# Optimization experiments

Hardware: AMD Instinct MI355X
Metric: run time of the kernel (lower is better)

## Reference

```python
import jax, jax.numpy as jnp
import numpy as np

N = 50000
E = 800000
IN_CH = 128
HID = 64
HEADS = 4
OUT_CH = 64
NEG_SLOPE = 0.2


def add_self_loops(edge_index, num_nodes):
    loops = jnp.arange(num_nodes, dtype=edge_index.dtype)
    src = jnp.concatenate([edge_index[0], loops])
    dst = jnp.concatenate([edge_index[1], loops])
    return src, dst


def gat_layer(x, src, dst, W, a_src, a_dst, b, heads, out_ch, concat):
    n = x.shape[0]
    h = (x @ W).reshape(n, heads, out_ch)              # [N,H,C]
    al_src = jnp.einsum('nhc,hc->nh', h, a_src)        # [N,H]
    al_dst = jnp.einsum('nhc,hc->nh', h, a_dst)        # [N,H]
    e = jax.nn.leaky_relu(al_src[src] + al_dst[dst], NEG_SLOPE)  # [Et,H]
    # segment softmax over incoming edges of each destination node
    m = jax.ops.segment_max(e, dst, num_segments=n)
    ex = jnp.exp(e - m[dst])
    denom = jax.ops.segment_sum(ex, dst, num_segments=n)
    alpha = ex / (denom[dst] + 1e-16)                  # [Et,H]
    msg = h[src] * alpha[:, :, None]                   # [Et,H,C]
    out = jax.ops.segment_sum(msg, dst, num_segments=n)  # [N,H,C]
    if concat:
        out = out.reshape(n, heads * out_ch)
    else:
        out = out.mean(axis=1)
    return out + b


def setup_inputs() -> dict:
    key = jax.random.key(0)
    ks = jax.random.split(key, 10)
    x = jax.random.normal(ks[0], (N, IN_CH), dtype=jnp.float32)
    edge_index = jax.random.randint(ks[1], (2, E), 0, N, dtype=jnp.int64)
    s1 = 1.0 / np.sqrt(IN_CH)
    W1 = jax.random.normal(ks[2], (IN_CH, HEADS * HID), dtype=jnp.float32) * s1
    a_src1 = jax.random.normal(ks[3], (HEADS, HID), dtype=jnp.float32) * 0.1
    a_dst1 = jax.random.normal(ks[4], (HEADS, HID), dtype=jnp.float32) * 0.1
    b1 = jnp.zeros((HEADS * HID,), dtype=jnp.float32)
    s2 = 1.0 / np.sqrt(HEADS * HID)
    W2 = jax.random.normal(ks[5], (HEADS * HID, OUT_CH), dtype=jnp.float32) * s2
    a_src2 = jax.random.normal(ks[6], (1, OUT_CH), dtype=jnp.float32) * 0.1
    a_dst2 = jax.random.normal(ks[7], (1, OUT_CH), dtype=jnp.float32) * 0.1
    b2 = jnp.zeros((OUT_CH,), dtype=jnp.float32)
    return {"x": x, "edge_index": edge_index, "W1": W1, "a_src1": a_src1,
            "a_dst1": a_dst1, "b1": b1, "W2": W2, "a_src2": a_src2,
            "a_dst2": a_dst2, "b2": b2}


def reference(x, edge_index, W1, a_src1, a_dst1, b1, W2, a_src2, a_dst2, b2):
    src, dst = add_self_loops(edge_index, x.shape[0])
    h = gat_layer(x, src, dst, W1, a_src1, a_dst1, b1, HEADS, HID, True)
    h = jax.nn.elu(h)
    h = gat_layer(h, src, dst, W2, a_src2, a_dst2, b2, 1, OUT_CH, False)
    return jax.nn.elu(h)
```

## Files before the change

### kernel.cpp

```cpp
#include <hip/hip_runtime.h>
#include <hip/hip_bf16.h>
#include <cstdint>
#include <cstddef>


typedef float f32x4 __attribute__((ext_vector_type(4)));
typedef __fp16 f16x8 __attribute__((ext_vector_type(8)));
typedef __fp16 f16x4 __attribute__((ext_vector_type(4)));

static __device__ __forceinline__ float lrelu02(float x) { return x > 0.f ? x : 0.2f * x; }
static __device__ __forceinline__ float eluf(float x)    { return x > 0.f ? x : __expf(x) - 1.f; }

__global__ void detect_kernel(const int* __restrict__ ei, int* __restrict__ flag, int e) {
    if (blockIdx.x == 0 && threadIdx.x == 0) {
        int zeros = 0;
        int m = e < 64 ? e : 64;
        for (int i = 0; i < m; ++i) if (ei[2 * i + 1] == 0) ++zeros;
        *flag = (zeros >= (m / 2 + 1)) ? 1 : 0;
    }
}

__global__ void convert_hist_kernel(const int* __restrict__ ei, const int* __restrict__ flag,
                                    int* __restrict__ es, int* __restrict__ deg, int e) {
    int i = blockIdx.x * 256 + threadIdx.x;
    if (i < e) {
        int f = *flag;
        int s = f ? ei[2 * i] : ei[i];
        int d = f ? ei[2 * (e + i)] : ei[e + i];
        es[i] = s;
        es[e + i] = d;
        atomicAdd(&deg[d], 1);
    }
}

__global__ __launch_bounds__(256) void scan_blocks_kernel(const int* __restrict__ deg,
                                                          int* __restrict__ loc,
                                                          int* __restrict__ bsum, int n) {
    __shared__ int wsum[4];
    int t = threadIdx.x, lane = t & 63, w = t >> 6;
    int base = blockIdx.x * 1024 + t * 4;
    int4 v = make_int4(0, 0, 0, 0);
    if (base + 3 < n) {
        v = *(const int4*)(deg + base);
        v.x += 1; v.y += 1; v.z += 1; v.w += 1;
    } else {
        if (base < n) v.x = deg[base] + 1;
        if (base + 1 < n) v.y = deg[base + 1] + 1;
        if (base + 2 < n) v.z = deg[base + 2] + 1;
        if (base + 3 < n) v.w = deg[base + 3] + 1;
    }
    int s = v.x + v.y + v.z + v.w;
    int incl = s;
    #pragma unroll
    for (int d = 1; d < 64; d <<= 1) { int o = __shfl_up(incl, d); if (lane >= d) incl += o; }
    if (lane == 63) wsum[w] = incl;
    __syncthreads();
    int woff = 0;
    for (int k = 0; k < w; ++k) woff += wsum[k];
    int excl = woff + incl - s;
    if (base < n) {
        int e0 = excl, e1 = e0 + v.x, e2 = e1 + v.y, e3 = e2 + v.z;
        loc[base] = e0;
        if (base + 1 < n) loc[base + 1] = e1;
        if (base + 2 < n) loc[base + 2] = e2;
        if (base + 3 < n) loc[base + 3] = e3;
    }
    if (t == 255) bsum[blockIdx.x] = woff + incl;
}

__global__ __launch_bounds__(256) void scan_sums_kernel(const int* __restrict__ bsum,
                                                        int* __restrict__ boff, int nb,
                                                        int* __restrict__ rowptr, int n) {
    __shared__ int ws[4];
    int t = threadIdx.x, lane = t & 63, w = t >> 6;
    int v = (t < nb) ? bsum[t] : 0;
    int incl = v;
    #pragma unroll
    for (int d = 1; d < 64; d <<= 1) { int o = __shfl_up(incl, d); if (lane >= d) incl += o; }
    if (lane == 63) ws[w] = incl;
    __syncthreads();
    int woff = 0;
    for (int k = 0; k < w; ++k) woff += ws[k];
    int excl = woff + incl - v;
    if (t < nb) boff[t] = excl;
    if (t == nb - 1) rowptr[n] = excl + v;
}

__global__ void scan_add_kernel(int* __restrict__ rowptr, const int* __restrict__ boff,
                                int* __restrict__ cursor, int n) {
    int i = blockIdx.x * 256 + threadIdx.x;
    if (i < n) {
        int v = rowptr[i] + boff[i >> 10];
        rowptr[i] = v;
        cursor[i] = v;
    }
}

__global__ void scatter_kernel(const int* __restrict__ src, const int* __restrict__ dst,
                               int* __restrict__ cursor, int* __restrict__ sidx,
                               int e, int et) {
    int i = blockIdx.x * blockDim.x + threadIdx.x;
    if (i < et) {
        int d, s;
        if (i < e) { d = dst[i]; s = src[i]; } else { d = s = i - e; }
        int pos = atomicAdd(&cursor[d], 1);
        sidx[pos] = s;
    }
}

__global__ __launch_bounds__(256) void gemm1_kernel(const float* __restrict__ A,
                                                    const float* __restrict__ B,
                                                    __fp16* __restrict__ C,
                                                    const float* __restrict__ a_src,
                                                    const float* __restrict__ a_dst,
                                                    float* __restrict__ als,
                                                    float* __restrict__ ald, int M) {
    constexpr int N = 256, K = 128;
    __shared__ __fp16 sm[17920];
    #define AS(r, c)  sm[(r) * 40 + (c)]
    #define BST(r, c) sm[2560 + (r) * 40 + (c)]
    #define CS(r, c)  sm[(r) * 264 + (c)]
    float* sa = (float*)(sm + 16896);
    float* sd = (float*)(sm + 17408);
    int t = threadIdx.x;
    int wv = t >> 6, l = t & 63;
    int lm = l & 15, kq = l >> 4;
    int bm = blockIdx.x * 64;
    sa[t] = a_src[t];
    sd[t] = a_dst[t];
    f32x4 zero = {0.f, 0.f, 0.f, 0.f};
    f32x4 acc[4][4] = {{zero, zero, zero, zero}, {zero, zero, zero, zero},
                       {zero, zero, zero, zero}, {zero, zero, zero, zero}};
    int arow = t >> 2, achunk = (t & 3) * 8;
    for (int k0 = 0; k0 < K; k0 += 32) {
        {
            int gr = bm + arow;
            f16x8 av;
            if (gr < M) {
                float4 a0 = *(const float4*)(A + (size_t)gr * K + k0 + achunk);
                float4 a1 = *(const float4*)(A + (size_t)gr * K + k0 + achunk + 4);
                av[0] = (__fp16)a0.x; av[1] = (__fp16)a0.y; av[2] = (__fp16)a0.z; av[3] = (__fp16)a0.w;
                av[4] = (__fp16)a1.x; av[5] = (__fp16)a1.y; av[6] = (__fp16)a1.z; av[7] = (__fp16)a1.w;
            } else { f16x8 z = {0,0,0,0,0,0,0,0}; av = z; }
            *(f16x8*)&AS(arow, achunk) = av;
        }
        {
            #pragma unroll
            for (int bc = 0; bc < 4; ++bc) {
                f16x8 bh;
                #pragma unroll
                for (int j = 0; j < 8; ++j)
                    bh[j] = (__fp16)B[(size_t)(k0 + bc * 8 + j) * N + t];
                *(f16x8*)&BST(t, bc * 8) = bh;
            }
        }
        __syncthreads();
        #pragma unroll
        for (int nt = 0; nt < 4; ++nt) {
            f16x8 bfrag = *(const f16x8*)&BST(wv * 64 + nt * 16 + lm, kq * 8);
            #pragma unroll
            for (int mt = 0; mt < 4; ++mt) {
                f16x8 afrag = *(const f16x8*)&AS(mt * 16 + lm, kq * 8);
                acc[mt][nt] = __builtin_amdgcn_mfma_f32_16x16x32_f16(afrag, bfrag, acc[mt][nt], 0, 0, 0);
            }
        }
        __syncthreads();
    }
    #pragma unroll
    for (int mt = 0; mt < 4; ++mt)
        #pragma unroll
        for (int nt = 0; nt < 4; ++nt)
            #pragma unroll
            for (int r = 0; r < 4; ++r)
                CS(mt * 16 + kq * 4 + r, wv * 64 + nt * 16 + lm) = (__fp16)acc[mt][nt][r];
    __syncthreads();
    {
        int row = t >> 2, head = t & 3;
        int gr = bm + row;
        f16x8 c[8];
        #pragma unroll
        for (int q = 0; q < 8; ++q) c[q] = *(const f16x8*)&CS(row, head * 64 + q * 8);
        float ps = 0.f, pd = 0.f;
        #pragma unroll
        for (int q = 0; q < 8; ++q)
            #pragma unroll
            for (int j = 0; j < 8; ++j) {
                float v = (float)c[q][j];
                ps += v * sa[head * 64 + q * 8 + j];
                pd += v * sd[head * 64 + q * 8 + j];
            }
        if (gr < M) {
            f16x8* gp = (f16x8*)(C + (size_t)gr * 256 + head * 64);
            #pragma unroll
            for (int q = 0; q < 8; ++q) gp[q] = c[q];
            als[gr * 4 + head] = ps;
            ald[gr * 4 + head] = pd;
        }
    }
    #undef AS
    #undef BST
    #undef CS
}

__global__ __launch_bounds__(256) void gemm2_kernel(const __fp16* __restrict__ A,
                                                    const float* __restrict__ B,
                                                    __fp16* __restrict__ C,
                                                    const float* __restrict__ a_src,
                                                    const float* __restrict__ a_dst,
                                                    float* __restrict__ als,
                                                    float* __restrict__ ald,
                                                    int M, int N, int K) {
    __shared__ __fp16 sm[5120];
    #define AS(r, c)  sm[(r) * 40 + (c)]
    #define BST(r, c) sm[2560 + (r) * 40 + (c)]
    #define CS(r, c)  sm[(r) * 72 + (c)]
    int t = threadIdx.x;
    int wv = t >> 6, l = t & 63;
    int bm = blockIdx.x * 64;
    int lm = l & 15, kq = l >> 4;
    f32x4 zero = {0.f, 0.f, 0.f, 0.f};
    f32x4 acc[4] = {zero, zero, zero, zero};
    int arow = t >> 2, achunk = (t & 3) * 8;
    int bnn = t & 63, bkc = (t >> 6) * 8;
    for (int k0 = 0; k0 < K; k0 += 32) {
        {
            int gr = bm + arow;
            f16x8 av;
            if (gr < M) av = *(const f16x8*)(A + (size_t)gr * K + k0 + achunk);
            else { f16x8 z = {0,0,0,0,0,0,0,0}; av = z; }
            *(f16x8*)&AS(arow, achunk) = av;
        }
        {
            f16x8 bh;
            #pragma unroll
            for (int j = 0; j < 8; ++j)
                bh[j] = (__fp16)B[(size_t)(k0 + bkc + j) * N + bnn];
            *(f16x8*)&BST(bnn, bkc) = bh;
        }
        __syncthreads();
        f16x8 bfrag = *(const f16x8*)&BST(wv * 16 + lm, kq * 8);
        #pragma unroll
        for (int mt = 0; mt < 4; ++mt) {
            f16x8 afrag = *(const f16x8*)&AS(mt * 16 + lm, kq * 8);
            acc[mt] = __builtin_amdgcn_mfma_f32_16x16x32_f16(afrag, bfrag, acc[mt], 0, 0, 0);
        }
        __syncthreads();
    }
    #pragma unroll
    for (int mt = 0; mt < 4; ++mt)
        #pragma unroll
        for (int r = 0; r < 4; ++r)
            CS(mt * 16 + kq * 4 + r, wv * 16 + lm) = (__fp16)acc[mt][r];
    __syncthreads();
    {
        int row = t >> 2, ch = (t & 3) * 16;
        int gr = bm + row;
        f16x8 c0 = *(const f16x8*)&CS(row, ch);
        f16x8 c1 = *(const f16x8*)&CS(row, ch + 8);
        if (gr < M) {
            f16x8* gp = (f16x8*)(C + (size_t)gr * N + ch);
            gp[0] = c0; gp[1] = c1;
        }
        float ps = 0.f, pd = 0.f;
        #pragma unroll
        for (int j = 0; j < 8; ++j) {
            float v0 = (float)c0[j], v1 = (float)c1[j];
            ps += v0 * a_src[ch + j] + v1 * a_src[ch + 8 + j];
            pd += v0 * a_dst[ch + j] + v1 * a_dst[ch + 8 + j];
        }
        ps += __shfl_down(ps, 2); ps += __shfl_down(ps, 1);
        pd += __shfl_down(pd, 2); pd += __shfl_down(pd, 1);
        if ((t & 3) == 0 && gr < M) {
            als[gr] = ps;
            ald[gr] = pd;
        }
    }
    #undef AS
    #undef BST
    #undef CS
}

__global__ __launch_bounds__(256) void agg1_kernel(const __fp16* __restrict__ h1,
                                                   const int* __restrict__ sidx,
                                                   const int* __restrict__ rowptr,
                                                   const float* __restrict__ als,
                                                   const float* __restrict__ ald,
                                                   const float* __restrict__ b1,
                                                   __fp16* __restrict__ x2, int n) {
    int t = threadIdx.x, wv = t >> 6, l = t & 63;
    int node = blockIdx.x * 4 + wv;
    if (node >= n) return;
    int le = l & 31, halfE = l >> 5;
    int head = le >> 3;
    float aldn = ald[node * 4 + head];
    int p0 = rowptr[node], p1 = rowptr[node + 1];
    float acc[8] = {0.f, 0.f, 0.f, 0.f, 0.f, 0.f, 0.f, 0.f};
    float accw = 0.f;
    auto body = [&](int p) {
        int s = sidx[p];
        float wt = __expf(lrelu02(als[s * 4 + head] + aldn));
        accw += wt;
        f16x8 r = *(const f16x8*)(h1 + (size_t)s * 256 + le * 8);
        #pragma unroll
        for (int j = 0; j < 8; ++j) acc[j] += wt * (float)r[j];
    };
    int p = p0 + halfE;
    for (; p + 2 < p1; p += 4) { body(p); body(p + 2); }
    if (p < p1) body(p);
    #pragma unroll
    for (int j = 0; j < 8; ++j) acc[j] += __shfl_down(acc[j], 32);
    accw += __shfl_down(accw, 32);
    if (l < 32) {
        float rd = 1.f / (accw + 1e-16f);
        f16x8 o;
        #pragma unroll
        for (int j = 0; j < 8; ++j) {
            float v = acc[j] * rd + b1[le * 8 + j];
            o[j] = (__fp16)eluf(v);
        }
        *(f16x8*)(x2 + (size_t)node * 256 + le * 8) = o;
    }
}

__global__ __launch_bounds__(256) void agg2_kernel(const __fp16* __restrict__ h2,
                                                   const int* __restrict__ sidx,
                                                   const int* __restrict__ rowptr,
                                                   const float* __restrict__ als,
                                                   const float* __restrict__ ald,
                                                   const float* __restrict__ b2,
                                                   float* __restrict__ out, int n) {
    int t = threadIdx.x, wv = t >> 6, l = t & 63;
    int node = blockIdx.x * 4 + wv;
    if (node >= n) return;
    int slot = l >> 3, cq = l & 7;
    float aldn = ald[node];
    int p0 = rowptr[node], p1 = rowptr[node + 1];
    float acc[8] = {0.f, 0.f, 0.f, 0.f, 0.f, 0.f, 0.f, 0.f};
    float accw = 0.f;
    auto body = [&](int p) {
        int s = sidx[p];
        float wt = __expf(lrelu02(als[s] + aldn));
        accw += wt;
        f16x8 r = *(const f16x8*)(h2 + (size_t)s * 64 + cq * 8);
        #pragma unroll
        for (int j = 0; j < 8; ++j) acc[j] += wt * (float)r[j];
    };
    int p = p0 + slot;
    for (; p + 8 < p1; p += 16) { body(p); body(p + 8); }
    if (p < p1) body(p);
    #pragma unroll
    for (int j = 0; j < 8; ++j) {
        acc[j] += __shfl_down(acc[j], 32);
        acc[j] += __shfl_down(acc[j], 16);
        acc[j] += __shfl_down(acc[j], 8);
    }
    accw += __shfl_down(accw, 32);
    accw += __shfl_down(accw, 16);
    accw += __shfl_down(accw, 8);
    if (l < 8) {
        float rd = 1.f / (accw + 1e-16f);
        float4 o0, o1;
        o0.x = eluf(acc[0] * rd + b2[cq * 8 + 0]);
        o0.y = eluf(acc[1] * rd + b2[cq * 8 + 1]);
        o0.z = eluf(acc[2] * rd + b2[cq * 8 + 2]);
        o0.w = eluf(acc[3] * rd + b2[cq * 8 + 3]);
        o1.x = eluf(acc[4] * rd + b2[cq * 8 + 4]);
        o1.y = eluf(acc[5] * rd + b2[cq * 8 + 5]);
        o1.z = eluf(acc[6] * rd + b2[cq * 8 + 6]);
        o1.w = eluf(acc[7] * rd + b2[cq * 8 + 7]);
        float4* gp = (float4*)(out + (size_t)node * 64 + cq * 8);
        gp[0] = o0; gp[1] = o1;
    }
}

extern "C" void kernel_launch(void* const* d_in, const int* in_sizes, int n_in,
                              void* d_out, int out_size, void* d_ws, size_t ws_size,
                              hipStream_t stream) {
    const float* x   = (const float*)d_in[0];
    const int*   ei  = (const int*)d_in[1];
    const float* W1  = (const float*)d_in[2];
    const float* as1 = (const float*)d_in[3];
    const float* ad1 = (const float*)d_in[4];
    const float* b1  = (const float*)d_in[5];
    const float* W2  = (const float*)d_in[6];
    const float* as2 = (const float*)d_in[7];
    const float* ad2 = (const float*)d_in[8];
    const float* b2  = (const float*)d_in[9];
    float* out = (float*)d_out;

    const int n  = in_sizes[0] / 128;
    const int e  = in_sizes[1] / 2;
    const int et = e + n;

    char* w = (char*)d_ws;
    size_t off = 0;
    auto take = [&](size_t bytes) -> void* {
        void* p = w + off;
        off = (off + bytes + 255) & ~(size_t)255;
        return p;
    };
    __fp16* h1h = (__fp16*)take((size_t)n * 256 * 2);
    __fp16* x2h = (__fp16*)take((size_t)n * 256 * 2);
    __fp16* h2h = (__fp16*)take((size_t)n * 64 * 2);
    float* al1s = (float*)take((size_t)n * 4 * 4);
    float* al1d = (float*)take((size_t)n * 4 * 4);
    float* al2s = (float*)take((size_t)n * 4);
    float* al2d = (float*)take((size_t)n * 4);
    int* deg    = (int*)take((size_t)(n + 1) * 4);
    int* rowptr = (int*)take((size_t)(n + 1) * 4);
    int* cursor = (int*)take((size_t)(n + 1) * 4);
    int* sidx   = (int*)take((size_t)et * 4);
    int* es     = (int*)take((size_t)2 * e * 4);
    int* bsum   = (int*)take(1024);
    int* boff   = (int*)take(1024);
    int* flag   = (int*)take(256);

    detect_kernel<<<1, 64, 0, stream>>>(ei, flag, e);
    hipMemsetAsync(deg, 0, (size_t)n * 4, stream);
    convert_hist_kernel<<<(e + 255) / 256, 256, 0, stream>>>(ei, flag, es, deg, e);
    const int* srcA = es;
    const int* dstA = es + e;

    int nb = (n + 1023) / 1024;
    scan_blocks_kernel<<<nb, 256, 0, stream>>>(deg, rowptr, bsum, n);
    scan_sums_kernel<<<1, 256, 0, stream>>>(bsum, boff, nb, rowptr, n);
    scan_add_kernel<<<(n + 255) / 256, 256, 0, stream>>>(rowptr, boff, cursor, n);
    scatter_kernel<<<(et + 255) / 256, 256, 0, stream>>>(srcA, dstA, cursor, sidx, e, et);

    const int mblocks = (n + 63) / 64;
    const int nodeblocks = (n + 3) / 4;

    gemm1_kernel<<<mblocks, 256, 0, stream>>>(x, W1, h1h, as1, ad1, al1s, al1d, n);
    agg1_kernel<<<nodeblocks, 256, 0, stream>>>(h1h, sidx, rowptr, al1s, al1d, b1, x2h, n);

    gemm2_kernel<<<mblocks, 256, 0, stream>>>(x2h, W2, h2h, as2, ad2, al2s, al2d, n, 64, 256);
    agg2_kernel<<<nodeblocks, 256, 0, stream>>>(h2h, sidx, rowptr, al2s, al2d, b2, out, n);
}
```

Baseline: 311.7 us.

## Pre-transpose weights to fp16, drop edge copy, widen GEMM K-tiles, unroll agg1

Adds a prep kernel that transposes and converts W1/W2 to fp16 once, so the GEMM kernels load B with contiguous vector loads instead of strided scalar float reads. Removes the intermediate es edge-array copy: the histogram and scatter kernels read edge_index directly using the layout flag. Doubles the GEMM K-tile to 64, halving the number of sync rounds, and unrolls the agg1 edge loop by 4. The detect kernel becomes a wave ballot. The extra launch and larger shared memory may reduce occupancy.

```diff
diff --git a/kernel.cpp b/kernel.cpp
--- a/kernel.cpp
+++ b/kernel.cpp
@@ -12,23 +12,19 @@
 static __device__ __forceinline__ float eluf(float x)    { return x > 0.f ? x : __expf(x) - 1.f; }
 
 __global__ void detect_kernel(const int* __restrict__ ei, int* __restrict__ flag, int e) {
-    if (blockIdx.x == 0 && threadIdx.x == 0) {
-        int zeros = 0;
-        int m = e < 64 ? e : 64;
-        for (int i = 0; i < m; ++i) if (ei[2 * i + 1] == 0) ++zeros;
-        *flag = (zeros >= (m / 2 + 1)) ? 1 : 0;
-    }
-}
-
-__global__ void convert_hist_kernel(const int* __restrict__ ei, const int* __restrict__ flag,
-                                    int* __restrict__ es, int* __restrict__ deg, int e) {
+    int lane = threadIdx.x;
+    int m = e < 64 ? e : 64;
+    int z = (lane < m && ei[2 * lane + 1] == 0) ? 1 : 0;
+    unsigned long long bal = __ballot(z);
+    if (lane == 0) *flag = (__popcll(bal) >= m / 2 + 1) ? 1 : 0;
+}
+
+__global__ void hist_kernel(const int* __restrict__ ei, const int* __restrict__ flag,
+                            int* __restrict__ deg, int e) {
     int i = blockIdx.x * 256 + threadIdx.x;
     if (i < e) {
         int f = *flag;
-        int s = f ? ei[2 * i] : ei[i];
         int d = f ? ei[2 * (e + i)] : ei[e + i];
-        es[i] = s;
-        es[e + i] = d;
         atomicAdd(&deg[d], 1);
     }
 }
@@ -96,32 +92,47 @@
     }
 }
 
-__global__ void scatter_kernel(const int* __restrict__ src, const int* __restrict__ dst,
+__global__ void scatter_kernel(const int* __restrict__ ei, const int* __restrict__ flag,
                                int* __restrict__ cursor, int* __restrict__ sidx,
                                int e, int et) {
-    int i = blockIdx.x * blockDim.x + threadIdx.x;
-    if (i < et) {
-        int d, s;
-        if (i < e) { d = dst[i]; s = src[i]; } else { d = s = i - e; }
-        int pos = atomicAdd(&cursor[d], 1);
-        sidx[pos] = s;
+    int i = blockIdx.x * 256 + threadIdx.x;
+    if (i >= et) return;
+    int s, d;
+    if (i < e) {
+        int f = *flag;
+        s = f ? ei[2 * i] : ei[i];
+        d = f ? ei[2 * (e + i)] : ei[e + i];
+    } else { s = d = i - e; }
+    int pos = atomicAdd(&cursor[d], 1);
+    sidx[pos] = s;
+}
+
+__global__ void prep_kernel(const float* __restrict__ W1, const float* __restrict__ W2,
+                            __fp16* __restrict__ w1t, __fp16* __restrict__ w2t) {
+    int i = blockIdx.x * 256 + threadIdx.x;
+    if (i < 32768) {
+        int nn = i >> 7, k = i & 127;
+        w1t[i] = (__fp16)W1[k * 256 + nn];
+    } else {
+        int j = i - 32768;
+        int nn = j >> 8, k = j & 255;
+        w2t[j] = (__fp16)W2[k * 64 + nn];
     }
 }
 
 __global__ __launch_bounds__(256) void gemm1_kernel(const float* __restrict__ A,
-                                                    const float* __restrict__ B,
+                                                    const __fp16* __restrict__ w1t,
                                                     __fp16* __restrict__ C,
                                                     const float* __restrict__ a_src,
                                                     const float* __restrict__ a_dst,
                                                     float* __restrict__ als,
                                                     float* __restrict__ ald, int M) {
-    constexpr int N = 256, K = 128;
-    __shared__ __fp16 sm[17920];
-    #define AS(r, c)  sm[(r) * 40 + (c)]
-    #define BST(r, c) sm[2560 + (r) * 40 + (c)]
+    __shared__ __fp16 sm[24064];
+    #define AS(r, c)  sm[(r) * 72 + (c)]
+    #define BST(r, c) sm[4608 + (r) * 72 + (c)]
     #define CS(r, c)  sm[(r) * 264 + (c)]
-    float* sa = (float*)(sm + 16896);
-    float* sd = (float*)(sm + 17408);
+    float* sa = (float*)(sm + 23040);
+    float* sd = (float*)(sm + 23552);
     int t = threadIdx.x;
     int wv = t >> 6, l = t & 63;
     int lm = l & 15, kq = l >> 4;
@@ -131,37 +142,46 @@
     f32x4 zero = {0.f, 0.f, 0.f, 0.f};
     f32x4 acc[4][4] = {{zero, zero, zero, zero}, {zero, zero, zero, zero},
                        {zero, zero, zero, zero}, {zero, zero, zero, zero}};
-    int arow = t >> 2, achunk = (t & 3) * 8;
-    for (int k0 = 0; k0 < K; k0 += 32) {
+    int arow = t >> 2, akp = (t & 3) * 16;
+    for (int k0 = 0; k0 < 128; k0 += 64) {
         {
             int gr = bm + arow;
-            f16x8 av;
+            f16x8 av0, av1;
             if (gr < M) {
-                float4 a0 = *(const float4*)(A + (size_t)gr * K + k0 + achunk);
-                float4 a1 = *(const float4*)(A + (size_t)gr * K + k0 + achunk + 4);
-                av[0] = (__fp16)a0.x; av[1] = (__fp16)a0.y; av[2] = (__fp16)a0.z; av[3] = (__fp16)a0.w;
-                av[4] = (__fp16)a1.x; av[5] = (__fp16)a1.y; av[6] = (__fp16)a1.z; av[7] = (__fp16)a1.w;
-            } else { f16x8 z = {0,0,0,0,0,0,0,0}; av = z; }
-            *(f16x8*)&AS(arow, achunk) = av;
+                const float* ap = A + (size_t)gr * 128 + k0 + akp;
+                float4 a0 = *(const float4*)(ap + 0);
+                float4 a1 = *(const float4*)(ap + 4);
+                float4 a2 = *(const float4*)(ap + 8);
+                float4 a3 = *(const float4*)(ap + 12);
+                av0[0] = (__fp16)a0.x; av0[1] = (__fp16)a0.y; av0[2] = (__fp16)a0.z; av0[3] = (__fp16)a0.w;
+                av0[4] = (__fp16)a1.x; av0[5] = (__fp16)a1.y; av0[6] = (__fp16)a1.z; av0[7] = (__fp16)a1.w;
+                av1[0] = (__fp16)a2.x; av1[1] = (__fp16)a2.y; av1[2] = (__fp16)a2.z; av1[3] = (__fp16)a2.w;
+                av1[4] = (__fp16)a3.x; av1[5] = (__fp16)a3.y; av1[6] = (__fp16)a3.z; av1[7] = (__fp16)a3.w;
+            } else {
+                f16x8 z = {0,0,0,0,0,0,0,0}; av0 = z; av1 = z;
+            }
+            *(f16x8*)&AS(arow, akp) = av0;
+            *(f16x8*)&AS(arow, akp + 8) = av1;
         }
         {
-            #pragma unroll
-            for (int bc = 0; bc < 4; ++bc) {
-                f16x8 bh;
+            const __fp16* bp = w1t + (size_t)t * 128 + k0;
+            #pragma unroll
+            for (int c = 0; c < 8; ++c)
+                *(f16x8*)&BST(t, c * 8) = *(const f16x8*)(bp + c * 8);
+        }
+        __syncthreads();
+        #pragma unroll
+        for (int ki = 0; ki < 2; ++ki) {
+            int kc = ki * 32 + kq * 8;
+            f16x8 af[4];
+            #pragma unroll
+            for (int mt = 0; mt < 4; ++mt) af[mt] = *(const f16x8*)&AS(mt * 16 + lm, kc);
+            #pragma unroll
+            for (int nt = 0; nt < 4; ++nt) {
+                f16x8 bfrag = *(const f16x8*)&BST(wv * 64 + nt * 16 + lm, kc);
                 #pragma unroll
-                for (int j = 0; j < 8; ++j)
-                    bh[j] = (__fp16)B[(size_t)(k0 + bc * 8 + j) * N + t];
-                *(f16x8*)&BST(t, bc * 8) = bh;
-            }
-        }
-        __syncthreads();
-        #pragma unroll
-        for (int nt = 0; nt < 4; ++nt) {
-            f16x8 bfrag = *(const f16x8*)&BST(wv * 64 + nt * 16 + lm, kq * 8);
-            #pragma unroll
-            for (int mt = 0; mt < 4; ++mt) {
-                f16x8 afrag = *(const f16x8*)&AS(mt * 16 + lm, kq * 8);
-                acc[mt][nt] = __builtin_amdgcn_mfma_f32_16x16x32_f16(afrag, bfrag, acc[mt][nt], 0, 0, 0);
+                for (int mt = 0; mt < 4; ++mt)
+                    acc[mt][nt] = __builtin_amdgcn_mfma_f32_16x16x32_f16(af[mt], bfrag, acc[mt][nt], 0, 0, 0);
             }
         }
         __syncthreads();
@@ -203,46 +223,51 @@
 }
 
 __global__ __launch_bounds__(256) void gemm2_kernel(const __fp16* __restrict__ A,
-                                                    const float* __restrict__ B,
+                                                    const __fp16* __restrict__ w2t,
                                                     __fp16* __restrict__ C,
                                                     const float* __restrict__ a_src,
                                                     const float* __restrict__ a_dst,
                                                     float* __restrict__ als,
-                                                    float* __restrict__ ald,
-                                                    int M, int N, int K) {
-    __shared__ __fp16 sm[5120];
-    #define AS(r, c)  sm[(r) * 40 + (c)]
-    #define BST(r, c) sm[2560 + (r) * 40 + (c)]
+                                                    float* __restrict__ ald, int M) {
+    __shared__ __fp16 sm[9216];
+    #define AS(r, c)  sm[(r) * 72 + (c)]
+    #define BST(r, c) sm[4608 + (r) * 72 + (c)]
     #define CS(r, c)  sm[(r) * 72 + (c)]
     int t = threadIdx.x;
     int wv = t >> 6, l = t & 63;
+    int lm = l & 15, kq = l >> 4;
     int bm = blockIdx.x * 64;
-    int lm = l & 15, kq = l >> 4;
     f32x4 zero = {0.f, 0.f, 0.f, 0.f};
     f32x4 acc[4] = {zero, zero, zero, zero};
-    int arow = t >> 2, achunk = (t & 3) * 8;
-    int bnn = t & 63, bkc = (t >> 6) * 8;
-    for (int k0 = 0; k0 < K; k0 += 32) {
+    int arow = t >> 2, akp = (t & 3) * 16;
+    int bn = t & 63, bkc = (t >> 6) * 16;
+    for (int k0 = 0; k0 < 256; k0 += 64) {
         {
             int gr = bm + arow;
-            f16x8 av;
-            if (gr < M) av = *(const f16x8*)(A + (size_t)gr * K + k0 + achunk);
-            else { f16x8 z = {0,0,0,0,0,0,0,0}; av = z; }
-            *(f16x8*)&AS(arow, achunk) = av;
+            f16x8 av0, av1;
+            if (gr < M) {
+                const __fp16* ap = A + (size_t)gr * 256 + k0 + akp;
+                av0 = *(const f16x8*)(ap);
+                av1 = *(const f16x8*)(ap + 8);
+            } else { f16x8 z = {0,0,0,0,0,0,0,0}; av0 = z; av1 = z; }
+            *(f16x8*)&AS(arow, akp) = av0;
+            *(f16x8*)&AS(arow, akp + 8) = av1;
         }
         {
-            f16x8 bh;
-            #pragma unroll
-            for (int j = 0; j < 8; ++j)
-                bh[j] = (__fp16)B[(size_t)(k0 + bkc + j) * N + bnn];
-            *(f16x8*)&BST(bnn, bkc) = bh;
+            const __fp16* bp = w2t + (size_t)bn * 256 + k0 + bkc;
+            *(f16x8*)&BST(bn, bkc) = *(const f16x8*)(bp);
+            *(f16x8*)&BST(bn, bkc + 8) = *(const f16x8*)(bp + 8);
         }
         __syncthreads();
-        f16x8 bfrag = *(const f16x8*)&BST(wv * 16 + lm, kq * 8);
-        #pragma unroll
-        for (int mt = 0; mt < 4; ++mt) {
-            f16x8 afrag = *(const f16x8*)&AS(mt * 16 + lm, kq * 8);
-            acc[mt] = __builtin_amdgcn_mfma_f32_16x16x32_f16(afrag, bfrag, acc[mt], 0, 0, 0);
+        #pragma unroll
+        for (int ki = 0; ki < 2; ++ki) {
+            int kc = ki * 32 + kq * 8;
+            f16x8 bfrag = *(const f16x8*)&BST(wv * 16 + lm, kc);
+            #pragma unroll
+            for (int mt = 0; mt < 4; ++mt) {
+                f16x8 afrag = *(const f16x8*)&AS(mt * 16 + lm, kc);
+                acc[mt] = __builtin_amdgcn_mfma_f32_16x16x32_f16(afrag, bfrag, acc[mt], 0, 0, 0);
+            }
         }
         __syncthreads();
     }
@@ -258,7 +283,7 @@
         f16x8 c0 = *(const f16x8*)&CS(row, ch);
         f16x8 c1 = *(const f16x8*)&CS(row, ch + 8);
         if (gr < M) {
-            f16x8* gp = (f16x8*)(C + (size_t)gr * N + ch);
+            f16x8* gp = (f16x8*)(C + (size_t)gr * 64 + ch);
             gp[0] = c0; gp[1] = c1;
         }
         float ps = 0.f, pd = 0.f;
@@ -305,8 +330,8 @@
         for (int j = 0; j < 8; ++j) acc[j] += wt * (float)r[j];
     };
     int p = p0 + halfE;
-    for (; p + 2 < p1; p += 4) { body(p); body(p + 2); }
-    if (p < p1) body(p);
+    for (; p + 6 < p1; p += 8) { body(p); body(p + 2); body(p + 4); body(p + 6); }
+    for (; p < p1; p += 2) body(p);
     #pragma unroll
     for (int j = 0; j < 8; ++j) acc[j] += __shfl_down(acc[j], 32);
     accw += __shfl_down(accw, 32);
@@ -402,6 +427,8 @@
     __fp16* h1h = (__fp16*)take((size_t)n * 256 * 2);
     __fp16* x2h = (__fp16*)take((size_t)n * 256 * 2);
     __fp16* h2h = (__fp16*)take((size_t)n * 64 * 2);
+    __fp16* w1t = (__fp16*)take((size_t)256 * 128 * 2);
+    __fp16* w2t = (__fp16*)take((size_t)64 * 256 * 2);
     float* al1s = (float*)take((size_t)n * 4 * 4);
     float* al1d = (float*)take((size_t)n * 4 * 4);
     float* al2s = (float*)take((size_t)n * 4);
@@ -410,29 +437,26 @@
     int* rowptr = (int*)take((size_t)(n + 1) * 4);
     int* cursor = (int*)take((size_t)(n + 1) * 4);
     int* sidx   = (int*)take((size_t)et * 4);
-    int* es     = (int*)take((size_t)2 * e * 4);
     int* bsum   = (int*)take(1024);
     int* boff   = (int*)take(1024);
     int* flag   = (int*)take(256);
 
     detect_kernel<<<1, 64, 0, stream>>>(ei, flag, e);
     hipMemsetAsync(deg, 0, (size_t)n * 4, stream);
-    convert_hist_kernel<<<(e + 255) / 256, 256, 0, stream>>>(ei, flag, es, deg, e);
-    const int* srcA = es;
-    const int* dstA = es + e;
-
+    prep_kernel<<<192, 256, 0, stream>>>(W1, W2, w1t, w2t);
+    hist_kernel<<<(e + 255) / 256, 256, 0, stream>>>(ei, flag, deg, e);
     int nb = (n + 1023) / 1024;
     scan_blocks_kernel<<<nb, 256, 0, stream>>>(deg, rowptr, bsum, n);
     scan_sums_kernel<<<1, 256, 0, stream>>>(bsum, boff, nb, rowptr, n);
     scan_add_kernel<<<(n + 255) / 256, 256, 0, stream>>>(rowptr, boff, cursor, n);
-    scatter_kernel<<<(et + 255) / 256, 256, 0, stream>>>(srcA, dstA, cursor, sidx, e, et);
+    scatter_kernel<<<(et + 255) / 256, 256, 0, stream>>>(ei, flag, cursor, sidx, e, et);
 
     const int mblocks = (n + 63) / 64;
     const int nodeblocks = (n + 3) / 4;
 
-    gemm1_kernel<<<mblocks, 256, 0, stream>>>(x, W1, h1h, as1, ad1, al1s, al1d, n);
+    gemm1_kernel<<<mblocks, 256, 0, stream>>>(x, w1t, h1h, as1, ad1, al1s, al1d, n);
     agg1_kernel<<<nodeblocks, 256, 0, stream>>>(h1h, sidx, rowptr, al1s, al1d, b1, x2h, n);
 
-    gemm2_kernel<<<mblocks, 256, 0, stream>>>(x2h, W2, h2h, as2, ad2, al2s, al2d, n, 64, 256);
+    gemm2_kernel<<<mblocks, 256, 0, stream>>>(x2h, w2t, h2h, as2, ad2, al2s, al2d, n);
     agg2_kernel<<<nodeblocks, 256, 0, stream>>>(h2h, sidx, rowptr, al2s, al2d, b2, out, n);
 }
```

After: 310.3 us. About the same (-0.5%).
